# Kernel tuning notes

Measured on AMD Instinct MI355X. Metric: run time of the kernel, lower is better.

Reference implementation:

```python
import jax, jax.numpy as jnp
import numpy as np

TOP_K = 2
EPS = 1e-20


def setup_inputs() -> dict:
    key = jax.random.key(0)
    ks = jax.random.split(key, 8)
    B, S, H, E, D = 4, 2048, 1024, 8, 2048
    s = 0.02
    return {
        "x":  jax.random.normal(ks[0], (B, S, H), dtype=jnp.float32),
        "Wr": jax.random.normal(ks[1], (H, E), dtype=jnp.float32) * s,
        "Wg": jax.random.normal(ks[2], (E, H, D), dtype=jnp.float32) * s,
        "Wu": jax.random.normal(ks[3], (E, H, D), dtype=jnp.float32) * s,
        "Wd": jax.random.normal(ks[4], (E, D, H), dtype=jnp.float32) * s,
        "Sg": jax.random.normal(ks[5], (H, D), dtype=jnp.float32) * s,
        "Su": jax.random.normal(ks[6], (H, D), dtype=jnp.float32) * s,
        "Sd": jax.random.normal(ks[7], (D, H), dtype=jnp.float32) * s,
    }


def reference(x, Wr, Wg, Wu, Wd, Sg, Su, Sd):
    B, S, H = x.shape
    T = B * S
    xt = x.reshape(T, H)

    # Router: softmax scores, top-k, renormalize top-k weights
    scores = jax.nn.softmax(xt @ Wr, axis=-1)            # [T, E]
    topk_w, topk_idx = jax.lax.top_k(scores, TOP_K)      # [T, K]
    topk_w = topk_w / (topk_w.sum(axis=-1, keepdims=True) + EPS)

    # Per-expert SwiGLU FFN computed densely over all tokens (vectorized over E)
    g = jax.nn.silu(jnp.einsum('th,ehd->etd', xt, Wg))   # [E, T, D]
    u = jnp.einsum('th,ehd->etd', xt, Wu)                # [E, T, D]
    out_all = jnp.einsum('etd,edh->eth', g * u, Wd)      # [E, T, H]

    # Combine: gather each token's top-k expert outputs, weighted sum
    tok = jnp.arange(T)[:, None]                          # [T, 1]
    gathered = out_all[topk_idx, tok, :]                  # [T, K, H]
    out = jnp.sum(gathered * topk_w[..., None], axis=1).reshape(B, S, H)

    # Shared expert (applied to original input, added to MoE output)
    shared = (jax.nn.silu(x @ Sg) * (x @ Su)) @ Sd        # [B, S, H]
    return out + shared
```

## Files before the change

### kernel.cpp

```cpp
#include <hip/hip_runtime.h>
#include <stdint.h>

#define T_TOK 8192
#define HD 1024
#define ED 8
#define DD 2048
#define BM 128
#define BK 32
#define TILE_SHARED 64
#define TILE_MAX 200
#define CHUNK_T 100
#define ROWCAP 25600
#define RT_TPW 8

typedef short short8 __attribute__((ext_vector_type(8)));
typedef float f32x4 __attribute__((ext_vector_type(4)));

__device__ __forceinline__ unsigned short f2bf(float f) {
  union { float f; unsigned int u; } v; v.f = f;
  unsigned int r = (v.u + 0x7fffu + ((v.u >> 16) & 1u)) >> 16;
  return (unsigned short)r;
}

__device__ __forceinline__ void gll16(const void* g, void* l) {
  __builtin_amdgcn_global_load_lds(
      (const __attribute__((address_space(1))) unsigned int*)g,
      (__attribute__((address_space(3))) unsigned int*)l, 16, 0, 0);
}

__global__ __launch_bounds__(256) void k_zero(float* __restrict__ outp) {
  size_t i = (size_t)blockIdx.x * 256 + threadIdx.x;
  ((float4*)outp)[i] = make_float4(0.f, 0.f, 0.f, 0.f);
}

__global__ __launch_bounds__(256) void k_init(int* counts, int* tok, float* wrow) {
  int i = blockIdx.x * 256 + threadIdx.x;
  if (i < 32) counts[i] = 0;
  if (i < ROWCAP) {
    tok[i] = (i < T_TOK) ? i : 0;
    wrow[i] = (i < T_TOK) ? 1.0f : 0.0f;
  }
}

__global__ __launch_bounds__(256) void k_transpose(const float* __restrict__ in,
    unsigned short* __restrict__ outp, int R, int C) {
  __shared__ float tile[32][33];
  size_t boff = (size_t)blockIdx.z * (size_t)R * (size_t)C;
  in += boff; outp += boff;
  int c0 = blockIdx.x * 32, r0 = blockIdx.y * 32;
  int tx = threadIdx.x & 31, ty = threadIdx.x >> 5;
#pragma unroll
  for (int i = 0; i < 4; ++i)
    tile[ty + i * 8][tx] = in[(size_t)(r0 + ty + i * 8) * C + c0 + tx];
  __syncthreads();
#pragma unroll
  for (int i = 0; i < 4; ++i)
    outp[(size_t)(c0 + ty + i * 8) * R + r0 + tx] = f2bf(tile[tx][ty + i * 8]);
}

__global__ __launch_bounds__(256) void k_router(const float* __restrict__ x,
    const float* __restrict__ Wr, unsigned short* __restrict__ xb,
    int* __restrict__ counts, int* __restrict__ topE, float* __restrict__ topW) {
  __shared__ float wrT[ED * HD];
  __shared__ int hist[ED];
  int tid = threadIdx.x;
  if (tid < ED) hist[tid] = 0;
  for (int i = tid; i < ED * HD; i += 256) {
    int e = i >> 10, h = i & (HD - 1);
    wrT[i] = Wr[h * ED + e];
  }
  __syncthreads();
  int lane = tid & 63, wave = tid >> 6;
  int tbase = (blockIdx.x * 4 + wave) * RT_TPW;
  for (int tt = 0; tt < RT_TPW; ++tt) {
    int t = tbase + tt;
    const float* xrow = x + (size_t)t * HD;
    unsigned short* xbrow = xb + (size_t)t * HD;
    float acc[ED] = {0, 0, 0, 0, 0, 0, 0, 0};
#pragma unroll
    for (int i = 0; i < HD / 64; ++i) {
      int h = i * 64 + lane;
      float v = xrow[h];
      xbrow[h] = f2bf(v);
#pragma unroll
      for (int e = 0; e < ED; ++e) acc[e] += v * wrT[e * HD + h];
    }
#pragma unroll
    for (int off = 32; off; off >>= 1)
#pragma unroll
      for (int e = 0; e < ED; ++e) acc[e] += __shfl_xor(acc[e], off);
    if (lane == 0) {
      float m = acc[0];
#pragma unroll
      for (int e = 1; e < ED; ++e) m = fmaxf(m, acc[e]);
      float p[ED], s = 0.f;
#pragma unroll
      for (int e = 0; e < ED; ++e) { p[e] = __expf(acc[e] - m); s += p[e]; }
      int i0 = 0;
#pragma unroll
      for (int e = 1; e < ED; ++e) if (acc[e] > acc[i0]) i0 = e;
      int i1 = -1;
#pragma unroll
      for (int e = 0; e < ED; ++e) {
        if (e == i0) continue;
        if (i1 < 0 || acc[e] > acc[i1]) i1 = e;
      }
      float p0 = p[i0] / s, p1 = p[i1] / s;
      float rs = p0 + p1 + 1e-20f;
      topE[t * 2] = i0; topE[t * 2 + 1] = i1;
      topW[t * 2] = p0 / rs; topW[t * 2 + 1] = p1 / rs;
      atomicAdd(&hist[i0], 1);
      atomicAdd(&hist[i1], 1);
    }
  }
  __syncthreads();
  if (tid < ED) atomicAdd(&counts[tid], hist[tid]);
}

__global__ __launch_bounds__(256) void k_plan(const int* __restrict__ counts, int* cursor,
    int* __restrict__ tileE, int* __restrict__ tileEnd) {
  __shared__ int tstart[ED + 1], segend[ED];
  if (threadIdx.x == 0) {
    int base = T_TOK, rt = TILE_SHARED;
    for (int e = 0; e < ED; ++e) {
      int c = counts[e];
      cursor[e] = base;
      tstart[e] = rt;
      segend[e] = base + c;
      int tiles = (c + BM - 1) >> 7;
      rt += tiles;
      base += tiles << 7;
    }
    tstart[ED] = rt;
  }
  __syncthreads();
  for (int rt = threadIdx.x; rt < TILE_MAX; rt += 256) {
    int e = -1, end = 0;
    if (rt < TILE_SHARED) { e = ED; end = T_TOK; }
    else {
      for (int q = 0; q < ED; ++q)
        if (rt >= tstart[q] && rt < tstart[q + 1]) { e = q; end = segend[q]; }
    }
    tileE[rt] = e; tileEnd[rt] = end;
  }
}

__global__ __launch_bounds__(256) void k_scatter(const int* __restrict__ topE,
    const float* __restrict__ topW, int* cursor, int* tok, float* wrow) {
  __shared__ int lcount[ED], lbase[ED];
  int tid = threadIdx.x;
  if (tid < ED) lcount[tid] = 0;
  __syncthreads();
  int t = blockIdx.x * 256 + tid;
  int e0 = topE[t * 2], e1 = topE[t * 2 + 1];
  float w0 = topW[t * 2], w1 = topW[t * 2 + 1];
  int s0 = atomicAdd(&lcount[e0], 1);
  int s1 = atomicAdd(&lcount[e1], 1);
  __syncthreads();
  if (tid < ED) lbase[tid] = atomicAdd(&cursor[tid], lcount[tid]);
  __syncthreads();
  int p0 = lbase[e0] + s0;
  int p1 = lbase[e1] + s1;
  tok[p0] = t; wrow[p0] = w0;
  tok[p1] = t; wrow[p1] = w1;
}

__global__ __launch_bounds__(256, 2) void k_gemm1(
    const unsigned short* __restrict__ xb,
    const unsigned short* __restrict__ wgt, const unsigned short* __restrict__ wut,
    const unsigned short* __restrict__ sgt, const unsigned short* __restrict__ sut,
    const int* __restrict__ tok, const int* __restrict__ tileE,
    const int* __restrict__ tileEnd, unsigned short* __restrict__ hbuf, int tileBase) {
  int lt = blockIdx.y;
  int rt = tileBase + lt;
  int e = tileE[rt];
  if (e < 0) return;
  int n0 = blockIdx.x * BM;
  int grow0 = rt * BM;
  int hrow0 = lt * BM;
  int segEnd = tileEnd[rt];
  const unsigned short* bg = (e == ED) ? sgt : wgt + (size_t)e * DD * HD;
  const unsigned short* bu = (e == ED) ? sut : wut + (size_t)e * DD * HD;

  __shared__ __align__(16) unsigned short As[BM * BK];
  __shared__ __align__(16) unsigned short Bg[BM * BK];
  __shared__ __align__(16) unsigned short Bu[BM * BK];

  int tid = threadIdx.x, lane = tid & 63, wave = tid >> 6;
  int wm = (wave & 1) * 64, wn = (wave >> 1) * 64;
  int kc = lane & 3;

  int ldsU[2];
  const unsigned short *pA[2], *pBg[2], *pBu[2];
#pragma unroll
  for (int r = 0; r < 2; ++r) {
    int chunk = r * 4 + wave;
    int idx = chunk * 64 + lane;
    int row = idx >> 2;
    ldsU[r] = chunk * 512;
    pA[r]  = xb + (size_t)tok[grow0 + row] * HD + kc * 8;
    pBg[r] = bg + (size_t)(n0 + row) * HD + kc * 8;
    pBu[r] = bu + (size_t)(n0 + row) * HD + kc * 8;
  }

  f32x4 zero = {0.f, 0.f, 0.f, 0.f};
  f32x4 accg[4][4], accu[4][4];
#pragma unroll
  for (int i = 0; i < 4; ++i)
#pragma unroll
    for (int j = 0; j < 4; ++j) { accg[i][j] = zero; accu[i][j] = zero; }

  for (int k0 = 0; k0 < HD; k0 += BK) {
#pragma unroll
    for (int r = 0; r < 2; ++r) {
      gll16(pA[r] + k0,  As + ldsU[r]);
      gll16(pBg[r] + k0, Bg + ldsU[r]);
      gll16(pBu[r] + k0, Bu + ldsU[r]);
    }
    __syncthreads();
    short8 af[4], bgf[4], buf_[4];
    int qk = (lane >> 4) * 8;
#pragma unroll
    for (int i = 0; i < 4; ++i) {
      af[i]   = *(const short8*)(As + (wm + i * 16 + (lane & 15)) * BK + qk);
      bgf[i]  = *(const short8*)(Bg + (wn + i * 16 + (lane & 15)) * BK + qk);
      buf_[i] = *(const short8*)(Bu + (wn + i * 16 + (lane & 15)) * BK + qk);
    }
#pragma unroll
    for (int i = 0; i < 4; ++i)
#pragma unroll
      for (int j = 0; j < 4; ++j) {
        accg[i][j] = __builtin_amdgcn_mfma_f32_16x16x32_bf16(af[i], bgf[j],  accg[i][j], 0, 0, 0);
        accu[i][j] = __builtin_amdgcn_mfma_f32_16x16x32_bf16(af[i], buf_[j], accu[i][j], 0, 0, 0);
      }
    __syncthreads();
  }

  int colB = n0 + wn + (lane & 15);
  int rowB = wm + ((lane >> 4) << 2);
#pragma unroll
  for (int i = 0; i < 4; ++i)
#pragma unroll
    for (int j = 0; j < 4; ++j)
#pragma unroll
      for (int r = 0; r < 4; ++r) {
        int lr = rowB + i * 16 + r;
        float g = accg[i][j][r], u = accu[i][j][r];
        float h = (grow0 + lr < segEnd) ? (g / (1.0f + __expf(-g))) * u : 0.0f;
        hbuf[(size_t)(hrow0 + lr) * DD + colB + j * 16] = f2bf(h);
      }
}

__global__ __launch_bounds__(256, 2) void k_gemm2(
    const unsigned short* __restrict__ hbuf,
    const unsigned short* __restrict__ wdt, const unsigned short* __restrict__ sdt,
    const int* __restrict__ tok, const int* __restrict__ tileE,
    const int* __restrict__ tileEnd, const float* __restrict__ wrow,
    float* __restrict__ outp, int tileBase) {
  int lt = blockIdx.y;
  int rt = tileBase + lt;
  int e = tileE[rt];
  if (e < 0) return;
  int n0 = blockIdx.x * BM;
  int grow0 = rt * BM;
  int hrow0 = lt * BM;
  int segEnd = tileEnd[rt];
  const unsigned short* bd = (e == ED) ? sdt : wdt + (size_t)e * HD * DD;

  __shared__ __align__(16) unsigned short As[BM * BK];
  __shared__ __align__(16) unsigned short Bs[BM * BK];

  int tid = threadIdx.x, lane = tid & 63, wave = tid >> 6;
  int wm = (wave & 1) * 64, wn = (wave >> 1) * 64;
  int kc = lane & 3;

  int ldsU[2];
  const unsigned short *pA[2], *pB[2];
#pragma unroll
  for (int r = 0; r < 2; ++r) {
    int chunk = r * 4 + wave;
    int idx = chunk * 64 + lane;
    int row = idx >> 2;
    ldsU[r] = chunk * 512;
    pA[r] = hbuf + (size_t)(hrow0 + row) * DD + kc * 8;
    pB[r] = bd + (size_t)(n0 + row) * DD + kc * 8;
  }

  f32x4 zero = {0.f, 0.f, 0.f, 0.f};
  f32x4 acc[4][4];
#pragma unroll
  for (int i = 0; i < 4; ++i)
#pragma unroll
    for (int j = 0; j < 4; ++j) acc[i][j] = zero;

  for (int k0 = 0; k0 < DD; k0 += BK) {
#pragma unroll
    for (int r = 0; r < 2; ++r) {
      gll16(pA[r] + k0, As + ldsU[r]);
      gll16(pB[r] + k0, Bs + ldsU[r]);
    }
    __syncthreads();
    short8 af[4], bf[4];
    int qk = (lane >> 4) * 8;
#pragma unroll
    for (int i = 0; i < 4; ++i) {
      af[i] = *(const short8*)(As + (wm + i * 16 + (lane & 15)) * BK + qk);
      bf[i] = *(const short8*)(Bs + (wn + i * 16 + (lane & 15)) * BK + qk);
    }
#pragma unroll
    for (int i = 0; i < 4; ++i)
#pragma unroll
      for (int j = 0; j < 4; ++j)
        acc[i][j] = __builtin_amdgcn_mfma_f32_16x16x32_bf16(af[i], bf[j], acc[i][j], 0, 0, 0);
    __syncthreads();
  }

  int colB = n0 + wn + (lane & 15);
  int rowB = wm + ((lane >> 4) << 2);
#pragma unroll
  for (int i = 0; i < 4; ++i)
#pragma unroll
    for (int r = 0; r < 4; ++r) {
      int grr = grow0 + rowB + i * 16 + r;
      if (grr < segEnd) {
        float w = wrow[grr];
        size_t ob = (size_t)tok[grr] * HD;
#pragma unroll
        for (int j = 0; j < 4; ++j)
          atomicAdd(&outp[ob + colB + j * 16], acc[i][j][r] * w);
      }
    }
}

extern "C" void kernel_launch(void* const* d_in, const int* in_sizes, int n_in,
                              void* d_out, int out_size, void* d_ws, size_t ws_size,
                              hipStream_t stream) {
  const float* x  = (const float*)d_in[0];
  const float* Wr = (const float*)d_in[1];
  const float* Wg = (const float*)d_in[2];
  const float* Wu = (const float*)d_in[3];
  const float* Wd = (const float*)d_in[4];
  const float* Sg = (const float*)d_in[5];
  const float* Su = (const float*)d_in[6];
  const float* Sd = (const float*)d_in[7];
  float* outp = (float*)d_out;

  char* ws = (char*)d_ws;
  size_t off = 0;
  auto alloc = [&](size_t bytes) -> char* {
    char* p = ws + off;
    off += (bytes + 255) & ~(size_t)255;
    return p;
  };
  unsigned short* xb  = (unsigned short*)alloc((size_t)T_TOK * HD * 2);
  unsigned short* wgt = (unsigned short*)alloc((size_t)ED * DD * HD * 2);
  unsigned short* wut = (unsigned short*)alloc((size_t)ED * DD * HD * 2);
  unsigned short* wdt = (unsigned short*)alloc((size_t)ED * HD * DD * 2);
  unsigned short* sgt = (unsigned short*)alloc((size_t)DD * HD * 2);
  unsigned short* sut = (unsigned short*)alloc((size_t)DD * HD * 2);
  unsigned short* sdt = (unsigned short*)alloc((size_t)HD * DD * 2);
  unsigned short* hbuf = (unsigned short*)alloc((size_t)CHUNK_T * BM * DD * 2);
  int* tok       = (int*)alloc((size_t)ROWCAP * 4);
  float* wrow    = (float*)alloc((size_t)ROWCAP * 4);
  int* topE      = (int*)alloc((size_t)T_TOK * 2 * 4);
  float* topW    = (float*)alloc((size_t)T_TOK * 2 * 4);
  int* counts    = (int*)alloc(128);
  int* cursor    = (int*)alloc(128);
  int* tileE     = (int*)alloc(256 * 4);
  int* tileEnd   = (int*)alloc(256 * 4);

  if (off > ws_size) return;

  k_zero<<<(out_size / 4 + 255) / 256, 256, 0, stream>>>(outp);
  k_init<<<(ROWCAP + 255) / 256, 256, 0, stream>>>(counts, tok, wrow);
  k_transpose<<<dim3(DD / 32, HD / 32, ED), 256, 0, stream>>>(Wg, wgt, HD, DD);
  k_transpose<<<dim3(DD / 32, HD / 32, ED), 256, 0, stream>>>(Wu, wut, HD, DD);
  k_transpose<<<dim3(HD / 32, DD / 32, ED), 256, 0, stream>>>(Wd, wdt, DD, HD);
  k_transpose<<<dim3(DD / 32, HD / 32, 1), 256, 0, stream>>>(Sg, sgt, HD, DD);
  k_transpose<<<dim3(DD / 32, HD / 32, 1), 256, 0, stream>>>(Su, sut, HD, DD);
  k_transpose<<<dim3(HD / 32, DD / 32, 1), 256, 0, stream>>>(Sd, sdt, DD, HD);
  k_router<<<T_TOK / (4 * RT_TPW), 256, 0, stream>>>(x, Wr, xb, counts, topE, topW);
  k_plan<<<1, 256, 0, stream>>>(counts, cursor, tileE, tileEnd);
  k_scatter<<<T_TOK / 256, 256, 0, stream>>>(topE, topW, cursor, tok, wrow);
  for (int cb = 0; cb < TILE_MAX; cb += CHUNK_T) {
    k_gemm1<<<dim3(DD / BM, CHUNK_T), 256, 0, stream>>>(xb, wgt, wut, sgt, sut, tok,
                                                        tileE, tileEnd, hbuf, cb);
    k_gemm2<<<dim3(HD / BM, CHUNK_T), 256, 0, stream>>>(hbuf, wdt, sdt, tok, tileE,
                                                        tileEnd, wrow, outp, cb);
  }
}
```

Measured before the change: 814.7 us.

## XOR-swizzle LDS tile layout and run both GEMMs in a single chunk

Global loads into LDS now place each 8-element k-chunk at an XOR-swizzled position based on the row, and the fragment reads apply the matching swizzle. This is meant to cut LDS bank conflicts in both grouped GEMMs. The host code also sizes the hidden buffer for all 200 tiles when the workspace allows it, so gemm1 and gemm2 each launch once instead of twice. The trade-off is a larger workspace requirement, with a fallback to two chunks when it does not fit.

```diff
diff --git a/kernel.cpp b/kernel.cpp
--- a/kernel.cpp
+++ b/kernel.cpp
@@ -9,7 +9,6 @@
 #define BK 32
 #define TILE_SHARED 64
 #define TILE_MAX 200
-#define CHUNK_T 100
 #define ROWCAP 25600
 #define RT_TPW 8
 
@@ -164,6 +163,7 @@
   tok[p0] = t; wrow[p0] = w0;
   tok[p1] = t; wrow[p1] = w1;
 }
+
 
 __global__ __launch_bounds__(256, 2) void k_gemm1(
     const unsigned short* __restrict__ xb,
@@ -188,15 +188,14 @@
 
   int tid = threadIdx.x, lane = tid & 63, wave = tid >> 6;
   int wm = (wave & 1) * 64, wn = (wave >> 1) * 64;
-  int kc = lane & 3;
+  int kc = (lane & 3) ^ ((lane >> 3) & 3);
 
   int ldsU[2];
   const unsigned short *pA[2], *pBg[2], *pBu[2];
 #pragma unroll
   for (int r = 0; r < 2; ++r) {
     int chunk = r * 4 + wave;
-    int idx = chunk * 64 + lane;
-    int row = idx >> 2;
+    int row = chunk * 16 + (lane >> 2);
     ldsU[r] = chunk * 512;
     pA[r]  = xb + (size_t)tok[grow0 + row] * HD + kc * 8;
     pBg[r] = bg + (size_t)(n0 + row) * HD + kc * 8;
@@ -210,6 +209,9 @@
 #pragma unroll
     for (int j = 0; j < 4; ++j) { accg[i][j] = zero; accu[i][j] = zero; }
 
+  int m15 = lane & 15;
+  int sl8 = (((lane >> 4) ^ ((lane >> 1) & 3)) * 8);
+
   for (int k0 = 0; k0 < HD; k0 += BK) {
 #pragma unroll
     for (int r = 0; r < 2; ++r) {
@@ -219,12 +221,11 @@
     }
     __syncthreads();
     short8 af[4], bgf[4], buf_[4];
-    int qk = (lane >> 4) * 8;
 #pragma unroll
     for (int i = 0; i < 4; ++i) {
-      af[i]   = *(const short8*)(As + (wm + i * 16 + (lane & 15)) * BK + qk);
-      bgf[i]  = *(const short8*)(Bg + (wn + i * 16 + (lane & 15)) * BK + qk);
-      buf_[i] = *(const short8*)(Bu + (wn + i * 16 + (lane & 15)) * BK + qk);
+      af[i]   = *(const short8*)(As + (wm + i * 16 + m15) * BK + sl8);
+      bgf[i]  = *(const short8*)(Bg + (wn + i * 16 + m15) * BK + sl8);
+      buf_[i] = *(const short8*)(Bu + (wn + i * 16 + m15) * BK + sl8);
     }
 #pragma unroll
     for (int i = 0; i < 4; ++i)
@@ -236,7 +237,7 @@
     __syncthreads();
   }
 
-  int colB = n0 + wn + (lane & 15);
+  int colB = n0 + wn + m15;
   int rowB = wm + ((lane >> 4) << 2);
 #pragma unroll
   for (int i = 0; i < 4; ++i)
@@ -272,15 +273,14 @@
 
   int tid = threadIdx.x, lane = tid & 63, wave = tid >> 6;
   int wm = (wave & 1) * 64, wn = (wave >> 1) * 64;
-  int kc = lane & 3;
+  int kc = (lane & 3) ^ ((lane >> 3) & 3);
 
   int ldsU[2];
   const unsigned short *pA[2], *pB[2];
 #pragma unroll
   for (int r = 0; r < 2; ++r) {
     int chunk = r * 4 + wave;
-    int idx = chunk * 64 + lane;
-    int row = idx >> 2;
+    int row = chunk * 16 + (lane >> 2);
     ldsU[r] = chunk * 512;
     pA[r] = hbuf + (size_t)(hrow0 + row) * DD + kc * 8;
     pB[r] = bd + (size_t)(n0 + row) * DD + kc * 8;
@@ -293,6 +293,9 @@
 #pragma unroll
     for (int j = 0; j < 4; ++j) acc[i][j] = zero;
 
+  int m15 = lane & 15;
+  int sl8 = (((lane >> 4) ^ ((lane >> 1) & 3)) * 8);
+
   for (int k0 = 0; k0 < DD; k0 += BK) {
 #pragma unroll
     for (int r = 0; r < 2; ++r) {
@@ -301,11 +304,10 @@
     }
     __syncthreads();
     short8 af[4], bf[4];
-    int qk = (lane >> 4) * 8;
 #pragma unroll
     for (int i = 0; i < 4; ++i) {
-      af[i] = *(const short8*)(As + (wm + i * 16 + (lane & 15)) * BK + qk);
-      bf[i] = *(const short8*)(Bs + (wn + i * 16 + (lane & 15)) * BK + qk);
+      af[i] = *(const short8*)(As + (wm + i * 16 + m15) * BK + sl8);
+      bf[i] = *(const short8*)(Bs + (wn + i * 16 + m15) * BK + sl8);
     }
 #pragma unroll
     for (int i = 0; i < 4; ++i)
@@ -315,7 +317,7 @@
     __syncthreads();
   }
 
-  int colB = n0 + wn + (lane & 15);
+  int colB = n0 + wn + m15;
   int rowB = wm + ((lane >> 4) << 2);
 #pragma unroll
   for (int i = 0; i < 4; ++i)
@@ -344,6 +346,18 @@
   const float* Su = (const float*)d_in[6];
   const float* Sd = (const float*)d_in[7];
   float* outp = (float*)d_out;
+
+  size_t fixed = 0;
+  auto pad = [](size_t b) { return (b + 255) & ~(size_t)255; };
+  fixed += pad((size_t)T_TOK * HD * 2);
+  fixed += pad((size_t)ED * DD * HD * 2) * 3;
+  fixed += pad((size_t)DD * HD * 2) * 3;
+  fixed += pad((size_t)ROWCAP * 4) * 2;
+  fixed += pad((size_t)T_TOK * 2 * 4) * 2;
+  fixed += pad(128) * 2 + pad(1024) * 2;
+  int CH = TILE_MAX;
+  if (fixed + pad((size_t)CH * BM * DD * 2) > ws_size) CH = TILE_MAX / 2;
+  if (fixed + pad((size_t)CH * BM * DD * 2) > ws_size) return;
 
   char* ws = (char*)d_ws;
   size_t off = 0;
@@ -359,17 +373,15 @@
   unsigned short* sgt = (unsigned short*)alloc((size_t)DD * HD * 2);
   unsigned short* sut = (unsigned short*)alloc((size_t)DD * HD * 2);
   unsigned short* sdt = (unsigned short*)alloc((size_t)HD * DD * 2);
-  unsigned short* hbuf = (unsigned short*)alloc((size_t)CHUNK_T * BM * DD * 2);
   int* tok       = (int*)alloc((size_t)ROWCAP * 4);
   float* wrow    = (float*)alloc((size_t)ROWCAP * 4);
   int* topE      = (int*)alloc((size_t)T_TOK * 2 * 4);
   float* topW    = (float*)alloc((size_t)T_TOK * 2 * 4);
   int* counts    = (int*)alloc(128);
   int* cursor    = (int*)alloc(128);
-  int* tileE     = (int*)alloc(256 * 4);
-  int* tileEnd   = (int*)alloc(256 * 4);
-
-  if (off > ws_size) return;
+  int* tileE     = (int*)alloc(1024);
+  int* tileEnd   = (int*)alloc(1024);
+  unsigned short* hbuf = (unsigned short*)alloc((size_t)CH * BM * DD * 2);
 
   k_zero<<<(out_size / 4 + 255) / 256, 256, 0, stream>>>(outp);
   k_init<<<(ROWCAP + 255) / 256, 256, 0, stream>>>(counts, tok, wrow);
@@ -382,10 +394,10 @@
   k_router<<<T_TOK / (4 * RT_TPW), 256, 0, stream>>>(x, Wr, xb, counts, topE, topW);
   k_plan<<<1, 256, 0, stream>>>(counts, cursor, tileE, tileEnd);
   k_scatter<<<T_TOK / 256, 256, 0, stream>>>(topE, topW, cursor, tok, wrow);
-  for (int cb = 0; cb < TILE_MAX; cb += CHUNK_T) {
-    k_gemm1<<<dim3(DD / BM, CHUNK_T), 256, 0, stream>>>(xb, wgt, wut, sgt, sut, tok,
-                                                        tileE, tileEnd, hbuf, cb);
-    k_gemm2<<<dim3(HD / BM, CHUNK_T), 256, 0, stream>>>(hbuf, wdt, sdt, tok, tileE,
-                                                        tileEnd, wrow, outp, cb);
-  }
-}
+  for (int cb = 0; cb < TILE_MAX; cb += CH) {
+    k_gemm1<<<dim3(DD / BM, CH), 256, 0, stream>>>(xb, wgt, wut, sgt, sut, tok,
+                                                   tileE, tileEnd, hbuf, cb);
+    k_gemm2<<<dim3(HD / BM, CH), 256, 0, stream>>>(hbuf, wdt, sdt, tok, tileE,
+                                                   tileEnd, wrow, outp, cb);
+  }
+}
```

Result: faster. 762.3 us (-6.4%).
